# Kernel optimization log

Hardware: AMD Instinct MI355X
Metric: run time of the kernel (lower is better)

The kernel has to match this reference:

```python
import jax, jax.numpy as jnp
import numpy as np

NUM_HEADS = 16
MAX_SEQ_LEN = 4096

def _rope_tables(head_dim, seq_len, dtype):
    inv_freq = 1.0 / (10000.0 ** (jnp.arange(0, head_dim, 2, dtype=jnp.float32) / head_dim))
    pos = jnp.arange(seq_len, dtype=jnp.float32)
    freqs = pos[:, None] * inv_freq[None, :]  # [S, hd/2]
    return jnp.cos(freqs).astype(dtype), jnp.sin(freqs).astype(dtype)

def _apply_rope(x, cos, sin):
    # x: [B, S, H, hd], interleaved even/odd pairs
    B, S, H, hd = x.shape
    xr = x.reshape(B, S, H, hd // 2, 2)
    xe, xo = xr[..., 0], xr[..., 1]
    c = cos[None, :, None, :]
    s = sin[None, :, None, :]
    ye = xe * c - xo * s
    yo = xe * s + xo * c
    return jnp.stack((ye, yo), axis=-1).reshape(B, S, H, hd)

def setup_inputs() -> dict:
    key = jax.random.key(0)
    k1, k2, k3 = jax.random.split(key, 3)
    B, S, D = 2, 2048, 2048
    x = jax.random.normal(k1, (B, S, D), dtype=jnp.float32)
    Wqkv = jax.random.normal(k2, (D, 3 * D), dtype=jnp.float32) * (D ** -0.5)
    Wo = jax.random.normal(k3, (D, D), dtype=jnp.float32) * (D ** -0.5)
    return {"x": x, "Wqkv": Wqkv, "Wo": Wo}

def reference(x, Wqkv, Wo):
    B, S, D = x.shape
    H = NUM_HEADS
    hd = D // H
    qkv = jnp.einsum('bsd,de->bse', x, Wqkv)  # [B,S,3D]
    q, k, v = jnp.split(qkv, 3, axis=-1)
    q = q.reshape(B, S, H, hd)
    k = k.reshape(B, S, H, hd)
    v = v.reshape(B, S, H, hd)
    cos, sin = _rope_tables(hd, S, x.dtype)
    q = _apply_rope(q, cos, sin)
    k = _apply_rope(k, cos, sin)
    scale = 1.0 / jnp.sqrt(jnp.asarray(hd, dtype=x.dtype))
    scores = jnp.einsum('bqhd,bkhd->bhqk', q, k) * scale  # [B,H,S,S]
    causal = jnp.tril(jnp.ones((S, S), dtype=bool))
    scores = jnp.where(causal[None, None], scores, jnp.asarray(-jnp.inf, dtype=scores.dtype))
    probs = jax.nn.softmax(scores, axis=-1)
    attn = jnp.einsum('bhqk,bkhd->bqhd', probs, v).reshape(B, S, D)
    return jnp.einsum('bsd,de->bse', attn, Wo)
```

## Files before the change

kernel.cpp:

```cpp
#include <hip/hip_runtime.h>
#include <cstddef>
#include <cstdint>
#include <math.h>

#define NB 2
#define NS 2048
#define ND 2048
#define NH 16
#define HD 128

typedef __attribute__((ext_vector_type(8))) short short8v;
typedef __attribute__((ext_vector_type(4))) float float4v;

#define MFMA16(A, B, C) __builtin_amdgcn_mfma_f32_16x16x32_bf16(A, B, C, 0, 0, 0)

__device__ __forceinline__ void split_bf16(float x, short& hi, short& lo) {
  unsigned u = __float_as_uint(x);
  unsigned hb = (u + 0x7FFFu + ((u >> 16) & 1u)) >> 16;
  float hif = __uint_as_float(hb << 16);
  float r = x - hif;
  unsigned ul = __float_as_uint(r);
  hi = (short)hb;
  lo = (short)((ul + 0x7FFFu + ((ul >> 16) & 1u)) >> 16);
}

__device__ __forceinline__ int pack2(short a, short b) {
  return (int)(unsigned short)a | ((int)(unsigned short)b << 16);
}

__global__ __launch_bounds__(256) void fused_prep_kernel(
    float2* __restrict__ tab,
    const float* __restrict__ Wqkv, short* __restrict__ wqh,
    short* __restrict__ wql,
    const float* __restrict__ Wo, short* __restrict__ woh,
    short* __restrict__ wol,
    const float* __restrict__ x, short* __restrict__ xh,
    short* __restrict__ xl) {
  __shared__ float T[32][33];
  const int tid = threadIdx.x;
  const int blk = blockIdx.x;
  if (blk < 512) {
    const int id = blk * 256 + tid;
    const int spos = id >> 6, p = id & 63;
    const float invf = powf(10000.f, -(float)p * (1.f / 64.f));
    float s, c;
    sincosf((float)spos * invf, &s, &c);
    tab[id] = make_float2(c, s);
  } else if (blk < 12800) {
    const int t = blk - 512;
    const int n0 = (t % 192) * 32, k0 = (t / 192) * 32;
    const int K = ND, N = 3 * ND;
    {
      const int r = tid >> 3, c4 = (tid & 7) << 2;
      float4 v = *(const float4*)&Wqkv[(size_t)(k0 + r) * N + n0 + c4];
      T[r][c4 + 0] = v.x;
      T[r][c4 + 1] = v.y;
      T[r][c4 + 2] = v.z;
      T[r][c4 + 3] = v.w;
    }
    __syncthreads();
    const int n = tid >> 3, k4 = (tid & 7) << 2;
    short h[4], l[4];
#pragma unroll
    for (int e = 0; e < 4; ++e) split_bf16(T[k4 + e][n], h[e], l[e]);
    const size_t off = (size_t)(n0 + n) * K + k0 + k4;
    *(int2*)&wqh[off] = make_int2(pack2(h[0], h[1]), pack2(h[2], h[3]));
    *(int2*)&wql[off] = make_int2(pack2(l[0], l[1]), pack2(l[2], l[3]));
  } else if (blk < 16896) {
    const int t = blk - 12800;
    const int n0 = (t % 64) * 32, k0 = (t / 64) * 32;
    const int K = ND, N = ND;
    {
      const int r = tid >> 3, c4 = (tid & 7) << 2;
      float4 v = *(const float4*)&Wo[(size_t)(k0 + r) * N + n0 + c4];
      T[r][c4 + 0] = v.x;
      T[r][c4 + 1] = v.y;
      T[r][c4 + 2] = v.z;
      T[r][c4 + 3] = v.w;
    }
    __syncthreads();
    const int n = tid >> 3, k4 = (tid & 7) << 2;
    short h[4], l[4];
#pragma unroll
    for (int e = 0; e < 4; ++e) split_bf16(T[k4 + e][n], h[e], l[e]);
    const size_t off = (size_t)(n0 + n) * K + k0 + k4;
    *(int2*)&woh[off] = make_int2(pack2(h[0], h[1]), pack2(h[2], h[3]));
    *(int2*)&wol[off] = make_int2(pack2(l[0], l[1]), pack2(l[2], l[3]));
  } else {
    const int n4 = NB * NS * ND / 4;
    for (int i = (blk - 16896) * 256 + tid; i < n4; i += 2048 * 256) {
      float4 v = ((const float4*)x)[i];
      short h0, l0, h1, l1, h2, l2, h3, l3;
      split_bf16(v.x, h0, l0);
      split_bf16(v.y, h1, l1);
      split_bf16(v.z, h2, l2);
      split_bf16(v.w, h3, l3);
      ((int2*)xh)[i] = make_int2(pack2(h0, h1), pack2(h2, h3));
      ((int2*)xl)[i] = make_int2(pack2(l0, l1), pack2(l2, l3));
    }
  }
}

__global__ __launch_bounds__(256) void rope_table_kernel(float2* tab) {
  const int id = blockIdx.x * 256 + threadIdx.x;
  const int spos = id >> 6, p = id & 63;
  const float invf = powf(10000.f, -(float)p * (1.f / 64.f));
  float s, c;
  sincosf((float)spos * invf, &s, &c);
  tab[id] = make_float2(c, s);
}

__global__ __launch_bounds__(256) void transpose_split_kernel(
    const float* __restrict__ W, short* __restrict__ Th, short* __restrict__ Tl,
    int K, int N) {
  __shared__ float T[32][33];
  const int tid = threadIdx.x;
  const int n0 = blockIdx.x * 32, k0 = blockIdx.y * 32;
  {
    const int r = tid >> 3, c4 = (tid & 7) << 2;
    float4 v = *(const float4*)&W[(size_t)(k0 + r) * N + n0 + c4];
    T[r][c4 + 0] = v.x;
    T[r][c4 + 1] = v.y;
    T[r][c4 + 2] = v.z;
    T[r][c4 + 3] = v.w;
  }
  __syncthreads();
  const int n = tid >> 3, k4 = (tid & 7) << 2;
  short h[4], l[4];
#pragma unroll
  for (int e = 0; e < 4; ++e) split_bf16(T[k4 + e][n], h[e], l[e]);
  const size_t off = (size_t)(n0 + n) * K + k0 + k4;
  *(int2*)&Th[off] = make_int2(pack2(h[0], h[1]), pack2(h[2], h[3]));
  *(int2*)&Tl[off] = make_int2(pack2(l[0], l[1]), pack2(l[2], l[3]));
}

template <bool ROPE, bool ASPLIT, int CHX, int CHY>
__global__ __launch_bounds__(256) void gemm_bf16x3_kernel(
    const float* __restrict__ Af, const short* __restrict__ Ahg,
    const short* __restrict__ Alg, const short* __restrict__ BTh,
    const short* __restrict__ BTl, float* __restrict__ C, int M, int N, int K,
    const float2* __restrict__ rope_tab) {
  __shared__ short Ah[128][40], Al[128][40];
  __shared__ short Bh[128][40], Bl[128][40];
  const int tid = threadIdx.x;
  const int wave = tid >> 6, lane = tid & 63;
  const int g = lane >> 4, r = lane & 15;
  const int wy = wave >> 1, wx = wave & 1;

  int bx = blockIdx.x, by = blockIdx.y;
  if (CHX > 0) {
    const int flat = by * gridDim.x + bx;
    const int xcd = flat & 7, idx = flat >> 3;
    bx = (xcd & 3) * CHX + idx % CHX;
    by = (xcd >> 2) * CHY + idx / CHX;
  }
  const int m0 = by * 128, n0 = bx * 128;
  const int wm = wy * 64, wn = wx * 64;

  const int ar = tid >> 1, ac = (tid & 1) << 4;

  const short* bhp = BTh + (size_t)(n0 + ar) * K + ac;
  const short* blp = BTl + (size_t)(n0 + ar) * K + ac;

  float4v acc[4][4];
#pragma unroll
  for (int i = 0; i < 4; ++i)
#pragma unroll
    for (int j = 0; j < 4; ++j) acc[i][j] = (float4v){0.f, 0.f, 0.f, 0.f};

  float4 a0, a1, a2, a3;
  int4 ah0, ah1, al0, al1;
  const float* aptr = nullptr;
  const short* ahp = nullptr;
  const short* alp = nullptr;
  if (ASPLIT) {
    ahp = Ahg + (size_t)(m0 + ar) * K + ac;
    alp = Alg + (size_t)(m0 + ar) * K + ac;
    ah0 = *(const int4*)(ahp);
    ah1 = *(const int4*)(ahp + 8);
    al0 = *(const int4*)(alp);
    al1 = *(const int4*)(alp + 8);
  } else {
    aptr = Af + (size_t)(m0 + ar) * K + ac;
    a0 = *(const float4*)(aptr);
    a1 = *(const float4*)(aptr + 4);
    a2 = *(const float4*)(aptr + 8);
    a3 = *(const float4*)(aptr + 12);
  }
  int4 bh0 = *(const int4*)(bhp);
  int4 bh1 = *(const int4*)(bhp + 8);
  int4 bl0 = *(const int4*)(blp);
  int4 bl1 = *(const int4*)(blp + 8);

  for (int k0 = 0; k0 < K; k0 += 32) {
    __syncthreads();
    if (ASPLIT) {
      *(int4*)&Ah[ar][ac] = ah0;
      *(int4*)&Ah[ar][ac + 8] = ah1;
      *(int4*)&Al[ar][ac] = al0;
      *(int4*)&Al[ar][ac + 8] = al1;
    } else {
      float xs[16] = {a0.x, a0.y, a0.z, a0.w, a1.x, a1.y, a1.z, a1.w,
                      a2.x, a2.y, a2.z, a2.w, a3.x, a3.y, a3.z, a3.w};
      short h[16], l[16];
#pragma unroll
      for (int e = 0; e < 16; ++e) split_bf16(xs[e], h[e], l[e]);
      *(int4*)&Ah[ar][ac] =
          make_int4(pack2(h[0], h[1]), pack2(h[2], h[3]), pack2(h[4], h[5]),
                    pack2(h[6], h[7]));
      *(int4*)&Ah[ar][ac + 8] =
          make_int4(pack2(h[8], h[9]), pack2(h[10], h[11]),
                    pack2(h[12], h[13]), pack2(h[14], h[15]));
      *(int4*)&Al[ar][ac] =
          make_int4(pack2(l[0], l[1]), pack2(l[2], l[3]), pack2(l[4], l[5]),
                    pack2(l[6], l[7]));
      *(int4*)&Al[ar][ac + 8] =
          make_int4(pack2(l[8], l[9]), pack2(l[10], l[11]),
                    pack2(l[12], l[13]), pack2(l[14], l[15]));
    }
    *(int4*)&Bh[ar][ac] = bh0;
    *(int4*)&Bh[ar][ac + 8] = bh1;
    *(int4*)&Bl[ar][ac] = bl0;
    *(int4*)&Bl[ar][ac + 8] = bl1;
    __syncthreads();
    if (k0 + 32 < K) {
      if (ASPLIT) {
        ah0 = *(const int4*)(ahp + k0 + 32);
        ah1 = *(const int4*)(ahp + k0 + 40);
        al0 = *(const int4*)(alp + k0 + 32);
        al1 = *(const int4*)(alp + k0 + 40);
      } else {
        const float* an = aptr + k0 + 32;
        a0 = *(const float4*)(an);
        a1 = *(const float4*)(an + 4);
        a2 = *(const float4*)(an + 8);
        a3 = *(const float4*)(an + 12);
      }
      bh0 = *(const int4*)(bhp + k0 + 32);
      bh1 = *(const int4*)(bhp + k0 + 40);
      bl0 = *(const int4*)(blp + k0 + 32);
      bl1 = *(const int4*)(blp + k0 + 40);
    }
    short8v afh[4], afl[4], bfh[4], bfl[4];
#pragma unroll
    for (int mi = 0; mi < 4; ++mi) {
      afh[mi] = *(const short8v*)&Ah[wm + mi * 16 + r][8 * g];
      afl[mi] = *(const short8v*)&Al[wm + mi * 16 + r][8 * g];
    }
#pragma unroll
    for (int nj = 0; nj < 4; ++nj) {
      bfh[nj] = *(const short8v*)&Bh[wn + nj * 16 + r][8 * g];
      bfl[nj] = *(const short8v*)&Bl[wn + nj * 16 + r][8 * g];
    }
#pragma unroll
    for (int mi = 0; mi < 4; ++mi)
#pragma unroll
      for (int nj = 0; nj < 4; ++nj) {
        acc[mi][nj] = MFMA16(afh[mi], bfh[nj], acc[mi][nj]);
        acc[mi][nj] = MFMA16(afh[mi], bfl[nj], acc[mi][nj]);
        acc[mi][nj] = MFMA16(afl[mi], bfh[nj], acc[mi][nj]);
      }
  }

  if (ROPE && n0 < 2 * ND) {
    int p[4];
#pragma unroll
    for (int nj = 0; nj < 4; ++nj)
      p[nj] = ((n0 + wn + nj * 16 + r) & (HD - 1)) >> 1;
    const bool even = (r & 1) == 0;
#pragma unroll
    for (int mi = 0; mi < 4; ++mi)
#pragma unroll
      for (int j = 0; j < 4; ++j) {
        const int spos = (m0 + wm + mi * 16 + 4 * g + j) & (NS - 1);
#pragma unroll
        for (int nj = 0; nj < 4; ++nj) {
          const float2 cs = rope_tab[spos * 64 + p[nj]];
          const float own = acc[mi][nj][j];
          const float oth = __shfl_xor(own, 1);
          acc[mi][nj][j] = even ? own * cs.x - oth * cs.y
                                : oth * cs.y + own * cs.x;
        }
      }
  }
#pragma unroll
  for (int mi = 0; mi < 4; ++mi)
#pragma unroll
    for (int j = 0; j < 4; ++j) {
      const size_t row = m0 + wm + mi * 16 + 4 * g + j;
      float* Crow = C + row * N + n0 + wn;
#pragma unroll
      for (int nj = 0; nj < 4; ++nj) Crow[nj * 16 + r] = acc[mi][nj][j];
    }
}

template <bool ROPE>
__global__ __launch_bounds__(256) void gemm_f32_kernel(
    const float* __restrict__ A, const float* __restrict__ Bm,
    float* __restrict__ C, int M, int N, int K) {
  __shared__ float As[16][132];
  __shared__ float Bs[16][132];
  const int tid = threadIdx.x;
  const int m0 = blockIdx.y * 128;
  const int n0 = blockIdx.x * 128;
  const int tr = tid >> 4;
  const int tc = tid & 15;
  const int la_r = tid >> 1;
  const int la_c = (tid & 1) << 3;
  const int lb_r = tid >> 4;
  const int lb_c = (tid & 15) << 3;

  const float* Aptr = A + (size_t)(m0 + la_r) * K + la_c;
  const float* Bptr = Bm + (size_t)lb_r * N + n0 + lb_c;

  float acc[8][8] = {};

  float4 av0 = *(const float4*)(Aptr);
  float4 av1 = *(const float4*)(Aptr + 4);
  float4 bv0 = *(const float4*)(Bptr);
  float4 bv1 = *(const float4*)(Bptr + 4);

  for (int k0 = 0; k0 < K; k0 += 16) {
    __syncthreads();
    As[la_c + 0][la_r] = av0.x;
    As[la_c + 1][la_r] = av0.y;
    As[la_c + 2][la_r] = av0.z;
    As[la_c + 3][la_r] = av0.w;
    As[la_c + 4][la_r] = av1.x;
    As[la_c + 5][la_r] = av1.y;
    As[la_c + 6][la_r] = av1.z;
    As[la_c + 7][la_r] = av1.w;
    *(float4*)&Bs[lb_r][lb_c] = bv0;
    *(float4*)&Bs[lb_r][lb_c + 4] = bv1;
    __syncthreads();
    if (k0 + 16 < K) {
      const float* An = Aptr + k0 + 16;
      const float* Bn = Bptr + (size_t)(k0 + 16) * N;
      av0 = *(const float4*)(An);
      av1 = *(const float4*)(An + 4);
      bv0 = *(const float4*)(Bn);
      bv1 = *(const float4*)(Bn + 4);
    }
#pragma unroll
    for (int kk = 0; kk < 16; ++kk) {
      float a[8], b[8];
      *(float4*)&a[0] = *(const float4*)&As[kk][tr << 2];
      *(float4*)&a[4] = *(const float4*)&As[kk][64 + (tr << 2)];
      *(float4*)&b[0] = *(const float4*)&Bs[kk][tc << 2];
      *(float4*)&b[4] = *(const float4*)&Bs[kk][64 + (tc << 2)];
#pragma unroll
      for (int i = 0; i < 8; ++i)
#pragma unroll
        for (int j = 0; j < 8; ++j) acc[i][j] = fmaf(a[i], b[j], acc[i][j]);
    }
  }

  if (ROPE) {
    if ((n0 >> 11) < 2) {
#pragma unroll
      for (int g = 0; g < 2; ++g) {
        const int col = n0 + g * 64 + (tc << 2);
        const int d0 = col & (HD - 1);
        const int p0 = d0 >> 1;
        const float invf0 = powf(10000.f, -(float)p0 * (1.f / 64.f));
        const float invf1 = powf(10000.f, -(float)(p0 + 1) * (1.f / 64.f));
#pragma unroll
        for (int rg = 0; rg < 2; ++rg) {
#pragma unroll
          for (int i = 0; i < 4; ++i) {
            const int row = m0 + rg * 64 + (tr << 2) + i;
            const int spos = row & (NS - 1);
            float s0, c0, s1, c1;
            sincosf((float)spos * invf0, &s0, &c0);
            sincosf((float)spos * invf1, &s1, &c1);
            float* ar2 = &acc[rg * 4 + i][g * 4];
            const float xe0 = ar2[0], xo0 = ar2[1];
            const float xe1 = ar2[2], xo1 = ar2[3];
            ar2[0] = xe0 * c0 - xo0 * s0;
            ar2[1] = xe0 * s0 + xo0 * c0;
            ar2[2] = xe1 * c1 - xo1 * s1;
            ar2[3] = xe1 * s1 + xo1 * c1;
          }
        }
      }
    }
  }
#pragma unroll
  for (int rg = 0; rg < 2; ++rg) {
#pragma unroll
    for (int i = 0; i < 4; ++i) {
      const size_t row = m0 + rg * 64 + (tr << 2) + i;
      float* Crow = C + row * N + n0;
      float4 v0 = make_float4(acc[rg * 4 + i][0], acc[rg * 4 + i][1],
                              acc[rg * 4 + i][2], acc[rg * 4 + i][3]);
      float4 v1 = make_float4(acc[rg * 4 + i][4], acc[rg * 4 + i][5],
                              acc[rg * 4 + i][6], acc[rg * 4 + i][7]);
      *(float4*)(Crow + (tc << 2)) = v0;
      *(float4*)(Crow + 64 + (tc << 2)) = v1;
    }
  }
}

template <bool SPLITOUT>
__global__ __launch_bounds__(512) void flash_attn_mfma(
    const float* __restrict__ qkv, float* __restrict__ O,
    short* __restrict__ Oh, short* __restrict__ Ol) {
  __shared__ short Khi[32][136];
  __shared__ short Klo[32][136];
  __shared__ short Vthi[128][40];
  __shared__ short Vtlo[128][40];
  __shared__ short Phi[8][16][40];
  __shared__ short Plo[8][16][40];

  const int tid = threadIdx.x;
  const int lane = tid & 63;
  const int wave = tid >> 6;
  const int g = lane >> 4;
  const int r = lane & 15;
  const int qtile = 15 - blockIdx.x;
  const int bh = blockIdx.y;
  const int b = bh >> 4, h = bh & 15;
  const int qb = qtile << 7;
  const int qw = qb + (wave << 4);
  const size_t row3d = 3 * ND;
  const float* base = qkv + (size_t)b * NS * row3d + (size_t)h * HD;
  const float* Kg = base + ND;
  const float* Vg = base + 2 * ND;

  const float scale = 0.088388347648318447f;
  const float* Qrow = base + (size_t)(qw + r) * row3d;
  short8v qhi[4], qlo[4];
#pragma unroll
  for (int hf = 0; hf < 4; ++hf) {
    const float* p = Qrow + 32 * hf + 8 * g;
    float4 x0 = *(const float4*)(p);
    float4 x1 = *(const float4*)(p + 4);
    float xs[8] = {x0.x, x0.y, x0.z, x0.w, x1.x, x1.y, x1.z, x1.w};
#pragma unroll
    for (int i = 0; i < 8; ++i) {
      short hi_, lo_;
      split_bf16(xs[i] * scale, hi_, lo_);
      qhi[hf][i] = hi_;
      qlo[hf][i] = lo_;
    }
  }

  float4v acc[8];
#pragma unroll
  for (int i = 0; i < 8; ++i) acc[i] = (float4v){0.f, 0.f, 0.f, 0.f};
  float m_run = -INFINITY;
  float l_run = 0.f;

  const int skv = tid >> 4;
  const int shd = (tid & 15) << 3;
  const int vkv = (tid & 15) << 1;
  const int vhd = (tid >> 4) << 2;
  const int ntiles = (qtile + 1) << 2;

  for (int t = 0; t < ntiles; ++t) {
    const int kvb = t << 5;
    __syncthreads();
    {
      const float* kr = Kg + (size_t)(kvb + skv) * row3d + shd;
#pragma unroll
      for (int u = 0; u < 2; ++u) {
        float4 v = *(const float4*)(kr + 4 * u);
        short h0, l0, h1, l1, h2, l2, h3, l3;
        split_bf16(v.x, h0, l0);
        split_bf16(v.y, h1, l1);
        split_bf16(v.z, h2, l2);
        split_bf16(v.w, h3, l3);
        *(int2*)&Khi[skv][shd + 4 * u] =
            make_int2(pack2(h0, h1), pack2(h2, h3));
        *(int2*)&Klo[skv][shd + 4 * u] =
            make_int2(pack2(l0, l1), pack2(l2, l3));
      }
    }
    {
      const float* v0p = Vg + (size_t)(kvb + vkv) * row3d + vhd;
      const float* v1p = v0p + row3d;
      float4 a0 = *(const float4*)(v0p);
      float4 b0 = *(const float4*)(v1p);
      float e0[4] = {a0.x, a0.y, a0.z, a0.w};
      float e1[4] = {b0.x, b0.y, b0.z, b0.w};
#pragma unroll
      for (int e = 0; e < 4; ++e) {
        short h0, l0, h1, l1;
        split_bf16(e0[e], h0, l0);
        split_bf16(e1[e], h1, l1);
        *(int*)&Vthi[vhd + e][vkv] = pack2(h0, h1);
        *(int*)&Vtlo[vhd + e][vkv] = pack2(l0, l1);
      }
    }
    __syncthreads();

    if (kvb <= qw + 15) {
      float4v s4[2];
#pragma unroll
      for (int f = 0; f < 2; ++f) s4[f] = (float4v){0.f, 0.f, 0.f, 0.f};
#pragma unroll
      for (int f = 0; f < 2; ++f) {
#pragma unroll
        for (int hf = 0; hf < 4; ++hf) {
          short8v ka = *(const short8v*)&Khi[16 * f + r][32 * hf + 8 * g];
          short8v kb = *(const short8v*)&Klo[16 * f + r][32 * hf + 8 * g];
          s4[f] = MFMA16(ka, qhi[hf], s4[f]);
          s4[f] = MFMA16(ka, qlo[hf], s4[f]);
          s4[f] = MFMA16(kb, qhi[hf], s4[f]);
        }
      }
      const int qglob = qw + r;
      if (kvb + 31 > qw) {
#pragma unroll
        for (int f = 0; f < 2; ++f)
#pragma unroll
          for (int j = 0; j < 4; ++j)
            if (kvb + 16 * f + 4 * g + j > qglob) s4[f][j] = -INFINITY;
      }
      float tmax = s4[0][0];
#pragma unroll
      for (int f = 0; f < 2; ++f)
#pragma unroll
        for (int j = 0; j < 4; ++j) tmax = fmaxf(tmax, s4[f][j]);
      tmax = fmaxf(tmax, __shfl_xor(tmax, 16));
      tmax = fmaxf(tmax, __shfl_xor(tmax, 32));
      const float mnew = fmaxf(m_run, tmax);
      const float alpha = __expf(m_run - mnew);
      float psum = 0.f;
      short ph[8], pl[8];
#pragma unroll
      for (int f = 0; f < 2; ++f)
#pragma unroll
        for (int j = 0; j < 4; ++j) {
          float p = __expf(s4[f][j] - mnew);
          psum += p;
          split_bf16(p, ph[4 * f + j], pl[4 * f + j]);
        }
      psum += __shfl_xor(psum, 16);
      psum += __shfl_xor(psum, 32);
      l_run = l_run * alpha + psum;
      m_run = mnew;
#pragma unroll
      for (int f = 0; f < 2; ++f) {
        *(int2*)&Phi[wave][r][16 * f + 4 * g] = make_int2(
            pack2(ph[4 * f + 0], ph[4 * f + 1]),
            pack2(ph[4 * f + 2], ph[4 * f + 3]));
        *(int2*)&Plo[wave][r][16 * f + 4 * g] = make_int2(
            pack2(pl[4 * f + 0], pl[4 * f + 1]),
            pack2(pl[4 * f + 2], pl[4 * f + 3]));
      }
      float aj[4];
#pragma unroll
      for (int j = 0; j < 4; ++j) aj[j] = __shfl(alpha, 4 * g + j);
#pragma unroll
      for (int hf = 0; hf < 8; ++hf)
#pragma unroll
        for (int j = 0; j < 4; ++j) acc[hf][j] *= aj[j];
      short8v pa = *(const short8v*)&Phi[wave][r][8 * g];
      short8v pb = *(const short8v*)&Plo[wave][r][8 * g];
#pragma unroll
      for (int hf = 0; hf < 8; ++hf) {
        short8v va = *(const short8v*)&Vthi[16 * hf + r][8 * g];
        short8v vb = *(const short8v*)&Vtlo[16 * hf + r][8 * g];
        acc[hf] = MFMA16(pa, va, acc[hf]);
        acc[hf] = MFMA16(pa, vb, acc[hf]);
        acc[hf] = MFMA16(pb, va, acc[hf]);
      }
    }
  }
  const float il = 1.f / l_run;
  float lj[4];
#pragma unroll
  for (int j = 0; j < 4; ++j) lj[j] = __shfl(il, 4 * g + j);
  const size_t obase = ((size_t)b * NS + qw) * ND + h * HD;
  if (SPLITOUT) {
    short* OhB = Oh + obase;
    short* OlB = Ol + obase;
#pragma unroll
    for (int hf = 0; hf < 8; ++hf)
#pragma unroll
      for (int j = 0; j < 4; ++j) {
        const float v = acc[hf][j] * lj[j];
        short h_, l_;
        split_bf16(v, h_, l_);
        const size_t idx = (size_t)(4 * g + j) * ND + 16 * hf + r;
        OhB[idx] = h_;
        OlB[idx] = l_;
      }
  } else {
    float* Ob = O + obase;
#pragma unroll
    for (int hf = 0; hf < 8; ++hf)
#pragma unroll
      for (int j = 0; j < 4; ++j)
        Ob[(size_t)(4 * g + j) * ND + 16 * hf + r] = acc[hf][j] * lj[j];
  }
}

extern "C" void kernel_launch(void* const* d_in, const int* in_sizes, int n_in,
                              void* d_out, int out_size, void* d_ws,
                              size_t ws_size, hipStream_t stream) {
  const float* x = (const float*)d_in[0];
  const float* Wqkv = (const float*)d_in[1];
  const float* Wo = (const float*)d_in[2];
  float* out = (float*)d_out;
  float* qkv = (float*)d_ws;
  float* attn = qkv + (size_t)NB * NS * 3 * ND;
  short* wqh = (short*)(attn + (size_t)NB * NS * ND);
  short* wql = wqh + (size_t)ND * 3 * ND;
  short* woh = wql + (size_t)ND * 3 * ND;
  short* wol = woh + (size_t)ND * ND;
  float2* tab = (float2*)(wol + (size_t)ND * ND);
  short* xh = (short*)(tab + (size_t)NS * 64);
  short* xl = xh + (size_t)NB * NS * ND;
  short* ath = xh;
  short* atl = xl;

  const size_t base_need =
      ((size_t)NB * NS * 3 * ND + (size_t)NB * NS * ND) * 4 +
      ((size_t)ND * 3 * ND + (size_t)ND * ND) * 2 * 2 + (size_t)NS * 64 * 8;
  const size_t full_need = base_need + (size_t)NB * NS * ND * 2 * 2;

  const int M = NB * NS;
  if (ws_size >= full_need) {
    fused_prep_kernel<<<18944, 256, 0, stream>>>(
        tab, Wqkv, wqh, wql, Wo, woh, wol, x, xh, xl);
    gemm_bf16x3_kernel<true, true, 12, 16>
        <<<dim3(3 * ND / 128, M / 128), 256, 0, stream>>>(
            nullptr, xh, xl, wqh, wql, qkv, M, 3 * ND, ND, tab);
    flash_attn_mfma<true><<<dim3(16, 32), 512, 0, stream>>>(
        qkv, nullptr, ath, atl);
    gemm_bf16x3_kernel<false, true, 4, 16>
        <<<dim3(ND / 128, M / 128), 256, 0, stream>>>(
            nullptr, ath, atl, woh, wol, out, M, ND, ND, tab);
  } else if (ws_size >= base_need) {
    rope_table_kernel<<<NS * 64 / 256, 256, 0, stream>>>(tab);
    transpose_split_kernel<<<dim3(3 * ND / 32, ND / 32), 256, 0, stream>>>(
        Wqkv, wqh, wql, ND, 3 * ND);
    transpose_split_kernel<<<dim3(ND / 32, ND / 32), 256, 0, stream>>>(
        Wo, woh, wol, ND, ND);
    gemm_bf16x3_kernel<true, false, 0, 0>
        <<<dim3(3 * ND / 128, M / 128), 256, 0, stream>>>(
            x, nullptr, nullptr, wqh, wql, qkv, M, 3 * ND, ND, tab);
    flash_attn_mfma<false><<<dim3(16, 32), 512, 0, stream>>>(
        qkv, attn, nullptr, nullptr);
    gemm_bf16x3_kernel<false, false, 0, 0>
        <<<dim3(ND / 128, M / 128), 256, 0, stream>>>(
            attn, nullptr, nullptr, woh, wol, out, M, ND, ND, tab);
  } else {
    gemm_f32_kernel<true>
        <<<dim3(3 * ND / 128, M / 128), 256, 0, stream>>>(
            x, Wqkv, qkv, M, 3 * ND, ND);
    flash_attn_mfma<false><<<dim3(16, 32), 512, 0, stream>>>(
        qkv, attn, nullptr, nullptr);
    gemm_f32_kernel<false>
        <<<dim3(ND / 128, M / 128), 256, 0, stream>>>(
            attn, Wo, out, M, ND, ND);
  }
}
```

Before: 699.8 us.

## Double-buffer LDS tiles in bf16x3 GEMM to use one barrier per k-step

```diff
diff --git a/kernel.cpp b/kernel.cpp
--- a/kernel.cpp
+++ b/kernel.cpp
@@ -140,8 +140,8 @@
     const short* __restrict__ Alg, const short* __restrict__ BTh,
     const short* __restrict__ BTl, float* __restrict__ C, int M, int N, int K,
     const float2* __restrict__ rope_tab) {
-  __shared__ short Ah[128][40], Al[128][40];
-  __shared__ short Bh[128][40], Bl[128][40];
+  __shared__ short Ah[2][128][40], Al[2][128][40];
+  __shared__ short Bh[2][128][40], Bl[2][128][40];
   const int tid = threadIdx.x;
   const int wave = tid >> 6, lane = tid & 63;
   const int g = lane >> 4, r = lane & 15;
@@ -170,88 +170,89 @@
 
   float4 a0, a1, a2, a3;
   int4 ah0, ah1, al0, al1;
+  int4 bh0, bh1, bl0, bl1;
   const float* aptr = nullptr;
   const short* ahp = nullptr;
   const short* alp = nullptr;
   if (ASPLIT) {
     ahp = Ahg + (size_t)(m0 + ar) * K + ac;
     alp = Alg + (size_t)(m0 + ar) * K + ac;
-    ah0 = *(const int4*)(ahp);
-    ah1 = *(const int4*)(ahp + 8);
-    al0 = *(const int4*)(alp);
-    al1 = *(const int4*)(alp + 8);
   } else {
     aptr = Af + (size_t)(m0 + ar) * K + ac;
-    a0 = *(const float4*)(aptr);
-    a1 = *(const float4*)(aptr + 4);
-    a2 = *(const float4*)(aptr + 8);
-    a3 = *(const float4*)(aptr + 12);
-  }
-  int4 bh0 = *(const int4*)(bhp);
-  int4 bh1 = *(const int4*)(bhp + 8);
-  int4 bl0 = *(const int4*)(blp);
-  int4 bl1 = *(const int4*)(blp + 8);
-
+  }
+
+#define LOADREGS(off)                          \
+  do {                                         \
+    if (ASPLIT) {                              \
+      ah0 = *(const int4*)(ahp + (off));       \
+      ah1 = *(const int4*)(ahp + (off) + 8);   \
+      al0 = *(const int4*)(alp + (off));       \
+      al1 = *(const int4*)(alp + (off) + 8);   \
+    } else {                                   \
+      const float* an = aptr + (off);          \
+      a0 = *(const float4*)(an);               \
+      a1 = *(const float4*)(an + 4);           \
+      a2 = *(const float4*)(an + 8);           \
+      a3 = *(const float4*)(an + 12);          \
+    }                                          \
+    bh0 = *(const int4*)(bhp + (off));         \
+    bh1 = *(const int4*)(bhp + (off) + 8);     \
+    bl0 = *(const int4*)(blp + (off));         \
+    bl1 = *(const int4*)(blp + (off) + 8);     \
+  } while (0)
+
+#define WRITEBUF(nb)                                                        \
+  do {                                                                      \
+    if (ASPLIT) {                                                           \
+      *(int4*)&Ah[nb][ar][ac] = ah0;                                        \
+      *(int4*)&Ah[nb][ar][ac + 8] = ah1;                                    \
+      *(int4*)&Al[nb][ar][ac] = al0;                                        \
+      *(int4*)&Al[nb][ar][ac + 8] = al1;                                    \
+    } else {                                                                \
+      float xs[16] = {a0.x, a0.y, a0.z, a0.w, a1.x, a1.y, a1.z, a1.w,       \
+                      a2.x, a2.y, a2.z, a2.w, a3.x, a3.y, a3.z, a3.w};      \
+      short h[16], l[16];                                                   \
+      for (int e = 0; e < 16; ++e) split_bf16(xs[e], h[e], l[e]);           \
+      *(int4*)&Ah[nb][ar][ac] =                                             \
+          make_int4(pack2(h[0], h[1]), pack2(h[2], h[3]),                   \
+                    pack2(h[4], h[5]), pack2(h[6], h[7]));                  \
+      *(int4*)&Ah[nb][ar][ac + 8] =                                         \
+          make_int4(pack2(h[8], h[9]), pack2(h[10], h[11]),                 \
+                    pack2(h[12], h[13]), pack2(h[14], h[15]));              \
+      *(int4*)&Al[nb][ar][ac] =                                             \
+          make_int4(pack2(l[0], l[1]), pack2(l[2], l[3]),                   \
+                    pack2(l[4], l[5]), pack2(l[6], l[7]));                  \
+      *(int4*)&Al[nb][ar][ac + 8] =                                         \
+          make_int4(pack2(l[8], l[9]), pack2(l[10], l[11]),                 \
+                    pack2(l[12], l[13]), pack2(l[14], l[15]));              \
+    }                                                                       \
+    *(int4*)&Bh[nb][ar][ac] = bh0;                                          \
+    *(int4*)&Bh[nb][ar][ac + 8] = bh1;                                      \
+    *(int4*)&Bl[nb][ar][ac] = bl0;                                          \
+    *(int4*)&Bl[nb][ar][ac + 8] = bl1;                                      \
+  } while (0)
+
+  LOADREGS(0);
+  WRITEBUF(0);
+  __syncthreads();
+  if (32 < K) LOADREGS(32);
+
+  int cur = 0;
   for (int k0 = 0; k0 < K; k0 += 32) {
-    __syncthreads();
-    if (ASPLIT) {
-      *(int4*)&Ah[ar][ac] = ah0;
-      *(int4*)&Ah[ar][ac + 8] = ah1;
-      *(int4*)&Al[ar][ac] = al0;
-      *(int4*)&Al[ar][ac + 8] = al1;
-    } else {
-      float xs[16] = {a0.x, a0.y, a0.z, a0.w, a1.x, a1.y, a1.z, a1.w,
-                      a2.x, a2.y, a2.z, a2.w, a3.x, a3.y, a3.z, a3.w};
-      short h[16], l[16];
-#pragma unroll
-      for (int e = 0; e < 16; ++e) split_bf16(xs[e], h[e], l[e]);
-      *(int4*)&Ah[ar][ac] =
-          make_int4(pack2(h[0], h[1]), pack2(h[2], h[3]), pack2(h[4], h[5]),
-                    pack2(h[6], h[7]));
-      *(int4*)&Ah[ar][ac + 8] =
-          make_int4(pack2(h[8], h[9]), pack2(h[10], h[11]),
-                    pack2(h[12], h[13]), pack2(h[14], h[15]));
-      *(int4*)&Al[ar][ac] =
-          make_int4(pack2(l[0], l[1]), pack2(l[2], l[3]), pack2(l[4], l[5]),
-                    pack2(l[6], l[7]));
-      *(int4*)&Al[ar][ac + 8] =
-          make_int4(pack2(l[8], l[9]), pack2(l[10], l[11]),
-                    pack2(l[12], l[13]), pack2(l[14], l[15]));
-    }
-    *(int4*)&Bh[ar][ac] = bh0;
-    *(int4*)&Bh[ar][ac + 8] = bh1;
-    *(int4*)&Bl[ar][ac] = bl0;
-    *(int4*)&Bl[ar][ac + 8] = bl1;
-    __syncthreads();
-    if (k0 + 32 < K) {
-      if (ASPLIT) {
-        ah0 = *(const int4*)(ahp + k0 + 32);
-        ah1 = *(const int4*)(ahp + k0 + 40);
-        al0 = *(const int4*)(alp + k0 + 32);
-        al1 = *(const int4*)(alp + k0 + 40);
-      } else {
-        const float* an = aptr + k0 + 32;
-        a0 = *(const float4*)(an);
-        a1 = *(const float4*)(an + 4);
-        a2 = *(const float4*)(an + 8);
-        a3 = *(const float4*)(an + 12);
-      }
-      bh0 = *(const int4*)(bhp + k0 + 32);
-      bh1 = *(const int4*)(bhp + k0 + 40);
-      bl0 = *(const int4*)(blp + k0 + 32);
-      bl1 = *(const int4*)(blp + k0 + 40);
-    }
+    const int nxt = cur ^ 1;
     short8v afh[4], afl[4], bfh[4], bfl[4];
 #pragma unroll
     for (int mi = 0; mi < 4; ++mi) {
-      afh[mi] = *(const short8v*)&Ah[wm + mi * 16 + r][8 * g];
-      afl[mi] = *(const short8v*)&Al[wm + mi * 16 + r][8 * g];
+      afh[mi] = *(const short8v*)&Ah[cur][wm + mi * 16 + r][8 * g];
+      afl[mi] = *(const short8v*)&Al[cur][wm + mi * 16 + r][8 * g];
     }
 #pragma unroll
     for (int nj = 0; nj < 4; ++nj) {
-      bfh[nj] = *(const short8v*)&Bh[wn + nj * 16 + r][8 * g];
-      bfl[nj] = *(const short8v*)&Bl[wn + nj * 16 + r][8 * g];
-    }
+      bfh[nj] = *(const short8v*)&Bh[cur][wn + nj * 16 + r][8 * g];
+      bfl[nj] = *(const short8v*)&Bl[cur][wn + nj * 16 + r][8 * g];
+    }
+    if (k0 + 32 < K) WRITEBUF(nxt);
+    if (k0 + 64 < K) LOADREGS(k0 + 64);
 #pragma unroll
     for (int mi = 0; mi < 4; ++mi)
 #pragma unroll
@@ -260,7 +261,11 @@
         acc[mi][nj] = MFMA16(afh[mi], bfl[nj], acc[mi][nj]);
         acc[mi][nj] = MFMA16(afl[mi], bfh[nj], acc[mi][nj]);
       }
-  }
+    __syncthreads();
+    cur = nxt;
+  }
+#undef LOADREGS
+#undef WRITEBUF
 
   if (ROPE && n0 < 2 * ND) {
     int p[4];
```

Result: no change. 712.4 us (+1.8%).

## Use 256x128 tile with 512 threads for QKV projection GEMM

Applied to the files above, without the earlier changes.

```diff
diff --git a/kernel.cpp b/kernel.cpp
--- a/kernel.cpp
+++ b/kernel.cpp
@@ -134,6 +134,119 @@
   *(int2*)&Tl[off] = make_int2(pack2(l[0], l[1]), pack2(l[2], l[3]));
 }
 
+__global__ __launch_bounds__(512) void gemm_bf16x3_256(
+    const short* __restrict__ Ahg, const short* __restrict__ Alg,
+    const short* __restrict__ BTh, const short* __restrict__ BTl,
+    float* __restrict__ C, int M, int N, int K,
+    const float2* __restrict__ rope_tab) {
+  __shared__ short Ah[256][40], Al[256][40];
+  __shared__ short Bh[128][40], Bl[128][40];
+  const int tid = threadIdx.x;
+  const int wave = tid >> 6, lane = tid & 63;
+  const int g = lane >> 4, r = lane & 15;
+  const int wy = wave >> 1, wx = wave & 1;
+
+  int bx = blockIdx.x, by = blockIdx.y;
+  {
+    const int flat = by * gridDim.x + bx;
+    const int xcd = flat & 7, idx = flat >> 3;
+    bx = (xcd & 3) * 12 + idx % 12;
+    by = (xcd >> 2) * 8 + idx / 12;
+  }
+  const int m0 = by * 256, n0 = bx * 128;
+  const int wm = wy * 64, wn = wx * 64;
+
+  const int ar = tid >> 1, ac = (tid & 1) << 4;
+  const int br = tid >> 2, bc = (tid & 3) << 3;
+
+  const short* ahp = Ahg + (size_t)(m0 + ar) * K + ac;
+  const short* alp = Alg + (size_t)(m0 + ar) * K + ac;
+  const short* bhp = BTh + (size_t)(n0 + br) * K + bc;
+  const short* blp = BTl + (size_t)(n0 + br) * K + bc;
+
+  float4v acc[4][4];
+#pragma unroll
+  for (int i = 0; i < 4; ++i)
+#pragma unroll
+    for (int j = 0; j < 4; ++j) acc[i][j] = (float4v){0.f, 0.f, 0.f, 0.f};
+
+  int4 ah0 = *(const int4*)(ahp);
+  int4 ah1 = *(const int4*)(ahp + 8);
+  int4 al0 = *(const int4*)(alp);
+  int4 al1 = *(const int4*)(alp + 8);
+  int4 bh0 = *(const int4*)(bhp);
+  int4 bl0 = *(const int4*)(blp);
+
+  for (int k0 = 0; k0 < K; k0 += 32) {
+    __syncthreads();
+    *(int4*)&Ah[ar][ac] = ah0;
+    *(int4*)&Ah[ar][ac + 8] = ah1;
+    *(int4*)&Al[ar][ac] = al0;
+    *(int4*)&Al[ar][ac + 8] = al1;
+    *(int4*)&Bh[br][bc] = bh0;
+    *(int4*)&Bl[br][bc] = bl0;
+    __syncthreads();
+    if (k0 + 32 < K) {
+      ah0 = *(const int4*)(ahp + k0 + 32);
+      ah1 = *(const int4*)(ahp + k0 + 40);
+      al0 = *(const int4*)(alp + k0 + 32);
+      al1 = *(const int4*)(alp + k0 + 40);
+      bh0 = *(const int4*)(bhp + k0 + 32);
+      bl0 = *(const int4*)(blp + k0 + 32);
+    }
+    short8v afh[4], afl[4], bfh[4], bfl[4];
+#pragma unroll
+    for (int mi = 0; mi < 4; ++mi) {
+      afh[mi] = *(const short8v*)&Ah[wm + mi * 16 + r][8 * g];
+      afl[mi] = *(const short8v*)&Al[wm + mi * 16 + r][8 * g];
+    }
+#pragma unroll
+    for (int nj = 0; nj < 4; ++nj) {
+      bfh[nj] = *(const short8v*)&Bh[wn + nj * 16 + r][8 * g];
+      bfl[nj] = *(const short8v*)&Bl[wn + nj * 16 + r][8 * g];
+    }
+#pragma unroll
+    for (int mi = 0; mi < 4; ++mi)
+#pragma unroll
+      for (int nj = 0; nj < 4; ++nj) {
+        acc[mi][nj] = MFMA16(afh[mi], bfh[nj], acc[mi][nj]);
+        acc[mi][nj] = MFMA16(afh[mi], bfl[nj], acc[mi][nj]);
+        acc[mi][nj] = MFMA16(afl[mi], bfh[nj], acc[mi][nj]);
+      }
+  }
+
+  if (n0 < 2 * ND) {
+    int p[4];
+#pragma unroll
+    for (int nj = 0; nj < 4; ++nj)
+      p[nj] = ((n0 + wn + nj * 16 + r) & (HD - 1)) >> 1;
+    const bool even = (r & 1) == 0;
+#pragma unroll
+    for (int mi = 0; mi < 4; ++mi)
+#pragma unroll
+      for (int j = 0; j < 4; ++j) {
+        const int spos = (m0 + wm + mi * 16 + 4 * g + j) & (NS - 1);
+#pragma unroll
+        for (int nj = 0; nj < 4; ++nj) {
+          const float2 cs = rope_tab[spos * 64 + p[nj]];
+          const float own = acc[mi][nj][j];
+          const float oth = __shfl_xor(own, 1);
+          acc[mi][nj][j] = even ? own * cs.x - oth * cs.y
+                                : oth * cs.y + own * cs.x;
+        }
+      }
+  }
+#pragma unroll
+  for (int mi = 0; mi < 4; ++mi)
+#pragma unroll
+    for (int j = 0; j < 4; ++j) {
+      const size_t row = m0 + wm + mi * 16 + 4 * g + j;
+      float* Crow = C + row * N + n0 + wn;
+#pragma unroll
+      for (int nj = 0; nj < 4; ++nj) Crow[nj * 16 + r] = acc[mi][nj][j];
+    }
+}
+
 template <bool ROPE, bool ASPLIT, int CHX, int CHY>
 __global__ __launch_bounds__(256) void gemm_bf16x3_kernel(
     const float* __restrict__ Af, const short* __restrict__ Ahg,
@@ -625,9 +738,8 @@
   if (ws_size >= full_need) {
     fused_prep_kernel<<<18944, 256, 0, stream>>>(
         tab, Wqkv, wqh, wql, Wo, woh, wol, x, xh, xl);
-    gemm_bf16x3_kernel<true, true, 12, 16>
-        <<<dim3(3 * ND / 128, M / 128), 256, 0, stream>>>(
-            nullptr, xh, xl, wqh, wql, qkv, M, 3 * ND, ND, tab);
+    gemm_bf16x3_256<<<dim3(3 * ND / 128, M / 256), 512, 0, stream>>>(
+        xh, xl, wqh, wql, qkv, M, 3 * ND, ND, tab);
     flash_attn_mfma<true><<<dim3(16, 32), 512, 0, stream>>>(
         qkv, nullptr, ath, atl);
     gemm_bf16x3_kernel<false, true, 4, 16>
```

After: 699.0 us (median of 2 runs). No clear change (-0.1%).

## Emit split bf16 hi/lo QKV from the projection GEMM and consume it in attention

Applied to the files above, without the earlier changes.

```diff
diff --git a/kernel.cpp b/kernel.cpp
--- a/kernel.cpp
+++ b/kernel.cpp
@@ -134,11 +134,12 @@
   *(int2*)&Tl[off] = make_int2(pack2(l[0], l[1]), pack2(l[2], l[3]));
 }
 
-template <bool ROPE, bool ASPLIT, int CHX, int CHY>
+template <bool ROPE, bool ASPLIT, bool SPLITC, int CHX, int CHY>
 __global__ __launch_bounds__(256) void gemm_bf16x3_kernel(
     const float* __restrict__ Af, const short* __restrict__ Ahg,
     const short* __restrict__ Alg, const short* __restrict__ BTh,
-    const short* __restrict__ BTl, float* __restrict__ C, int M, int N, int K,
+    const short* __restrict__ BTl, float* __restrict__ C,
+    short* __restrict__ Ch, short* __restrict__ Cl, int M, int N, int K,
     const float2* __restrict__ rope_tab) {
   __shared__ short Ah[128][40], Al[128][40];
   __shared__ short Bh[128][40], Bl[128][40];
@@ -288,9 +289,21 @@
 #pragma unroll
     for (int j = 0; j < 4; ++j) {
       const size_t row = m0 + wm + mi * 16 + 4 * g + j;
-      float* Crow = C + row * N + n0 + wn;
-#pragma unroll
-      for (int nj = 0; nj < 4; ++nj) Crow[nj * 16 + r] = acc[mi][nj][j];
+      if (SPLITC) {
+        short* Chr = Ch + row * N + n0 + wn;
+        short* Clr = Cl + row * N + n0 + wn;
+#pragma unroll
+        for (int nj = 0; nj < 4; ++nj) {
+          short h_, l_;
+          split_bf16(acc[mi][nj][j], h_, l_);
+          Chr[nj * 16 + r] = h_;
+          Clr[nj * 16 + r] = l_;
+        }
+      } else {
+        float* Crow = C + row * N + n0 + wn;
+#pragma unroll
+        for (int nj = 0; nj < 4; ++nj) Crow[nj * 16 + r] = acc[mi][nj][j];
+      }
     }
 }
 
@@ -401,9 +414,10 @@
   }
 }
 
-template <bool SPLITOUT>
+template <bool SPLITIN, bool SPLITOUT>
 __global__ __launch_bounds__(512) void flash_attn_mfma(
-    const float* __restrict__ qkv, float* __restrict__ O,
+    const float* __restrict__ qkv, const short* __restrict__ qkvh,
+    const short* __restrict__ qkvl, float* __restrict__ O,
     short* __restrict__ Oh, short* __restrict__ Ol) {
   __shared__ short Khi[32][136];
   __shared__ short Klo[32][136];
@@ -423,25 +437,35 @@
   const int qb = qtile << 7;
   const int qw = qb + (wave << 4);
   const size_t row3d = 3 * ND;
-  const float* base = qkv + (size_t)b * NS * row3d + (size_t)h * HD;
-  const float* Kg = base + ND;
-  const float* Vg = base + 2 * ND;
+  const size_t boff = (size_t)b * NS * row3d + (size_t)h * HD;
+  const float* base = SPLITIN ? nullptr : qkv + boff;
+  const short* baseh = SPLITIN ? qkvh + boff : nullptr;
+  const short* basel = SPLITIN ? qkvl + boff : nullptr;
 
   const float scale = 0.088388347648318447f;
-  const float* Qrow = base + (size_t)(qw + r) * row3d;
   short8v qhi[4], qlo[4];
-#pragma unroll
-  for (int hf = 0; hf < 4; ++hf) {
-    const float* p = Qrow + 32 * hf + 8 * g;
-    float4 x0 = *(const float4*)(p);
-    float4 x1 = *(const float4*)(p + 4);
-    float xs[8] = {x0.x, x0.y, x0.z, x0.w, x1.x, x1.y, x1.z, x1.w};
-#pragma unroll
-    for (int i = 0; i < 8; ++i) {
-      short hi_, lo_;
-      split_bf16(xs[i] * scale, hi_, lo_);
-      qhi[hf][i] = hi_;
-      qlo[hf][i] = lo_;
+  if (SPLITIN) {
+    const size_t qoff = (size_t)(qw + r) * row3d;
+#pragma unroll
+    for (int hf = 0; hf < 4; ++hf) {
+      qhi[hf] = *(const short8v*)&baseh[qoff + 32 * hf + 8 * g];
+      qlo[hf] = *(const short8v*)&basel[qoff + 32 * hf + 8 * g];
+    }
+  } else {
+    const float* Qrow = base + (size_t)(qw + r) * row3d;
+#pragma unroll
+    for (int hf = 0; hf < 4; ++hf) {
+      const float* p = Qrow + 32 * hf + 8 * g;
+      float4 x0 = *(const float4*)(p);
+      float4 x1 = *(const float4*)(p + 4);
+      float xs[8] = {x0.x, x0.y, x0.z, x0.w, x1.x, x1.y, x1.z, x1.w};
+#pragma unroll
+      for (int i = 0; i < 8; ++i) {
+        short hi_, lo_;
+        split_bf16(xs[i] * scale, hi_, lo_);
+        qhi[hf][i] = hi_;
+        qlo[hf][i] = lo_;
+      }
     }
   }
 
@@ -460,36 +484,56 @@
   for (int t = 0; t < ntiles; ++t) {
     const int kvb = t << 5;
     __syncthreads();
-    {
-      const float* kr = Kg + (size_t)(kvb + skv) * row3d + shd;
-#pragma unroll
-      for (int u = 0; u < 2; ++u) {
-        float4 v = *(const float4*)(kr + 4 * u);
-        short h0, l0, h1, l1, h2, l2, h3, l3;
-        split_bf16(v.x, h0, l0);
-        split_bf16(v.y, h1, l1);
-        split_bf16(v.z, h2, l2);
-        split_bf16(v.w, h3, l3);
-        *(int2*)&Khi[skv][shd + 4 * u] =
-            make_int2(pack2(h0, h1), pack2(h2, h3));
-        *(int2*)&Klo[skv][shd + 4 * u] =
-            make_int2(pack2(l0, l1), pack2(l2, l3));
-      }
-    }
-    {
-      const float* v0p = Vg + (size_t)(kvb + vkv) * row3d + vhd;
-      const float* v1p = v0p + row3d;
-      float4 a0 = *(const float4*)(v0p);
-      float4 b0 = *(const float4*)(v1p);
-      float e0[4] = {a0.x, a0.y, a0.z, a0.w};
-      float e1[4] = {b0.x, b0.y, b0.z, b0.w};
-#pragma unroll
-      for (int e = 0; e < 4; ++e) {
-        short h0, l0, h1, l1;
-        split_bf16(e0[e], h0, l0);
-        split_bf16(e1[e], h1, l1);
-        *(int*)&Vthi[vhd + e][vkv] = pack2(h0, h1);
-        *(int*)&Vtlo[vhd + e][vkv] = pack2(l0, l1);
+    if (SPLITIN) {
+      {
+        const size_t koff = (size_t)(kvb + skv) * row3d + ND + shd;
+        *(int4*)&Khi[skv][shd] = *(const int4*)&baseh[koff];
+        *(int4*)&Klo[skv][shd] = *(const int4*)&basel[koff];
+      }
+      {
+        const size_t voff = (size_t)(kvb + vkv) * row3d + 2 * ND + vhd;
+        const short* v0h = &baseh[voff];
+        const short* v1h = v0h + row3d;
+        const short* v0l = &basel[voff];
+        const short* v1l = v0l + row3d;
+#pragma unroll
+        for (int e = 0; e < 4; ++e) {
+          *(int*)&Vthi[vhd + e][vkv] = pack2(v0h[e], v1h[e]);
+          *(int*)&Vtlo[vhd + e][vkv] = pack2(v0l[e], v1l[e]);
+        }
+      }
+    } else {
+      {
+        const float* kr = base + ND + (size_t)(kvb + skv) * row3d + shd;
+#pragma unroll
+        for (int u = 0; u < 2; ++u) {
+          float4 v = *(const float4*)(kr + 4 * u);
+          short h0, l0, h1, l1, h2, l2, h3, l3;
+          split_bf16(v.x, h0, l0);
+          split_bf16(v.y, h1, l1);
+          split_bf16(v.z, h2, l2);
+          split_bf16(v.w, h3, l3);
+          *(int2*)&Khi[skv][shd + 4 * u] =
+              make_int2(pack2(h0, h1), pack2(h2, h3));
+          *(int2*)&Klo[skv][shd + 4 * u] =
+              make_int2(pack2(l0, l1), pack2(l2, l3));
+        }
+      }
+      {
+        const float* v0p = base + 2 * ND + (size_t)(kvb + vkv) * row3d + vhd;
+        const float* v1p = v0p + row3d;
+        float4 a0 = *(const float4*)(v0p);
+        float4 b0 = *(const float4*)(v1p);
+        float e0[4] = {a0.x, a0.y, a0.z, a0.w};
+        float e1[4] = {b0.x, b0.y, b0.z, b0.w};
+#pragma unroll
+        for (int e = 0; e < 4; ++e) {
+          short h0, l0, h1, l1;
+          split_bf16(e0[e], h0, l0);
+          split_bf16(e1[e], h1, l1);
+          *(int*)&Vthi[vhd + e][vkv] = pack2(h0, h1);
+          *(int*)&Vtlo[vhd + e][vkv] = pack2(l0, l1);
+        }
       }
     }
     __syncthreads();
@@ -508,6 +552,12 @@
           s4[f] = MFMA16(ka, qlo[hf], s4[f]);
           s4[f] = MFMA16(kb, qhi[hf], s4[f]);
         }
+      }
+      if (SPLITIN) {
+#pragma unroll
+        for (int f = 0; f < 2; ++f)
+#pragma unroll
+          for (int j = 0; j < 4; ++j) s4[f][j] *= scale;
       }
       const int qglob = qw + r;
       if (kvb + 31 > qw) {
@@ -605,6 +655,8 @@
   const float* Wo = (const float*)d_in[2];
   float* out = (float*)d_out;
   float* qkv = (float*)d_ws;
+  short* qkvh = (short*)d_ws;
+  short* qkvl = qkvh + (size_t)NB * NS * 3 * ND;
   float* attn = qkv + (size_t)NB * NS * 3 * ND;
   short* wqh = (short*)(attn + (size_t)NB * NS * ND);
   short* wql = wqh + (size_t)ND * 3 * ND;
@@ -625,34 +677,38 @@
   if (ws_size >= full_need) {
     fused_prep_kernel<<<18944, 256, 0, stream>>>(
         tab, Wqkv, wqh, wql, Wo, woh, wol, x, xh, xl);
-    gemm_bf16x3_kernel<true, true, 12, 16>
+    gemm_bf16x3_kernel<true, true, true, 12, 16>
         <<<dim3(3 * ND / 128, M / 128), 256, 0, stream>>>(
-            nullptr, xh, xl, wqh, wql, qkv, M, 3 * ND, ND, tab);
-    flash_attn_mfma<true><<<dim3(16, 32), 512, 0, stream>>>(
-        qkv, nullptr, ath, atl);
-    gemm_bf16x3_kernel<false, true, 4, 16>
+            nullptr, xh, xl, wqh, wql, nullptr, qkvh, qkvl, M, 3 * ND, ND,
+            tab);
+    flash_attn_mfma<true, true><<<dim3(16, 32), 512, 0, stream>>>(
+        nullptr, qkvh, qkvl, nullptr, ath, atl);
+    gemm_bf16x3_kernel<false, true, false, 4, 16>
         <<<dim3(ND / 128, M / 128), 256, 0, stream>>>(
-            nullptr, ath, atl, woh, wol, out, M, ND, ND, tab);
+            nullptr, ath, atl, woh, wol, out, nullptr, nullptr, M, ND, ND,
+            tab);
   } else if (ws_size >= base_need) {
     rope_table_kernel<<<NS * 64 / 256, 256, 0, stream>>>(tab);
     transpose_split_kernel<<<dim3(3 * ND / 32, ND / 32), 256, 0, stream>>>(
         Wqkv, wqh, wql, ND, 3 * ND);
     transpose_split_kernel<<<dim3(ND / 32, ND / 32), 256, 0, stream>>>(
         Wo, woh, wol, ND, ND);
-    gemm_bf16x3_kernel<true, false, 0, 0>
+    gemm_bf16x3_kernel<true, false, false, 0, 0>
         <<<dim3(3 * ND / 128, M / 128), 256, 0, stream>>>(
-            x, nullptr, nullptr, wqh, wql, qkv, M, 3 * ND, ND, tab);
-    flash_attn_mfma<false><<<dim3(16, 32), 512, 0, stream>>>(
-        qkv, attn, nullptr, nullptr);
-    gemm_bf16x3_kernel<false, false, 0, 0>
+            x, nullptr, nullptr, wqh, wql, qkv, nullptr, nullptr, M, 3 * ND,
+            ND, tab);
+    flash_attn_mfma<false, false><<<dim3(16, 32), 512, 0, stream>>>(
+        qkv, nullptr, nullptr, attn, nullptr, nullptr);
+    gemm_bf16x3_kernel<false, false, false, 0, 0>
         <<<dim3(ND / 128, M / 128), 256, 0, stream>>>(
-            attn, nullptr, nullptr, woh, wol, out, M, ND, ND, tab);
+            attn, nullptr, nullptr, woh, wol, out, nullptr, nullptr, M, ND,
+            ND, tab);
   } else {
     gemm_f32_kernel<true>
         <<<dim3(3 * ND / 128, M / 128), 256, 0, stream>>>(
             x, Wqkv, qkv, M, 3 * ND, ND);
-    flash_attn_mfma<false><<<dim3(16, 32), 512, 0, stream>>>(
-        qkv, attn, nullptr, nullptr);
+    flash_attn_mfma<false, false><<<dim3(16, 32), 512, 0, stream>>>(
+        qkv, nullptr, nullptr, attn, nullptr, nullptr);
     gemm_f32_kernel<false>
         <<<dim3(ND / 128, M / 128), 256, 0, stream>>>(
             attn, Wo, out, M, ND, ND);
```

After: 743.2 us. +6.2%, slower.
